# Performance work log

Measured on AMD Instinct MI355X. Metric: run time of the kernel, lower is better.

Reference implementation:

```python
import jax, jax.numpy as jnp
import numpy as np

B, N, C = 32, 512, 1024
H = 16
D = C // H  # 64
MAX_SEQ = 512
BASE = 10000.0


def _rope_tables(n, d):
    # sin/cos tables of shape (n, d//2), matching the torch RoPE buffer math
    position = jnp.arange(n, dtype=jnp.float32)[:, None]
    div_term = jnp.exp(jnp.arange(0, d, 2, dtype=jnp.float32) * (-np.log(BASE) / d))
    ang = position * div_term
    return jnp.sin(ang), jnp.cos(ang)


def _apply_rope(x, sin, cos):
    # x: (B, H, N, D); sin/cos: (N, D//2)
    x1 = x[..., ::2]
    x2 = x[..., 1::2]
    out = jnp.stack([x1 * cos - x2 * sin, x1 * sin + x2 * cos], axis=-1)
    return out.reshape(*x.shape[:-1], -1)


def setup_inputs() -> dict:
    key = jax.random.key(0)
    k1, k2, k3, k4, k5 = jax.random.split(key, 5)
    s = 0.02
    return {
        "x": jax.random.normal(k1, (B, N, C), dtype=jnp.float32),
        "w_qkv": jax.random.normal(k2, (3 * C, C), dtype=jnp.float32) * s,
        "b_qkv": jax.random.normal(k3, (3 * C,), dtype=jnp.float32) * s,
        "w_lepe": jax.random.normal(k4, (C, 1, 3), dtype=jnp.float32) * s,
        "b_lepe": jax.random.normal(k5, (C,), dtype=jnp.float32) * s,
    }


def reference(x, w_qkv, b_qkv, w_lepe, b_lepe):
    b, n, c = x.shape
    scale = 1.0 / np.sqrt(D)
    sin, cos = _rope_tables(n, D)

    # fused QKV projection: (B,N,3C) -> (3,B,H,N,D)
    qkv = (x @ w_qkv.T + b_qkv).reshape(b, n, 3, H, D).transpose(2, 0, 3, 1, 4)
    q, k, v = qkv[0], qkv[1], qkv[2]

    # elu + 1 feature map
    q = jax.nn.elu(q) + 1.0
    k = jax.nn.elu(k) + 1.0

    # RoPE on q/k
    q = _apply_rope(q, sin, cos)
    k = _apply_rope(k, sin, cos)

    # explicit softmax attention
    attn = jnp.einsum('bhnd,bhmd->bhnm', q, k) * scale
    attn = jax.nn.softmax(attn, axis=-1)
    attn_out = jnp.einsum('bhnm,bhmd->bhnd', attn, v)  # (B,H,N,D)
    attn_out = attn_out.transpose(0, 2, 1, 3).reshape(b, n, c)

    # LePE: depthwise conv1d (k=3, pad=1, groups=C) on v reshaped to (B,C,N)
    v_conv = v.transpose(0, 2, 1, 3).reshape(b, n, c).transpose(0, 2, 1)
    lepe = jax.lax.conv_general_dilated(
        v_conv, w_lepe, window_strides=(1,), padding=((1, 1),),
        dimension_numbers=('NCH', 'OIH', 'NCH'), feature_group_count=c,
    ) + b_lepe[None, :, None]
    lepe = lepe.transpose(0, 2, 1)

    return attn_out + lepe
```

## Files before the change

### kernel.cpp

```cpp
#include <hip/hip_runtime.h>
#include <stdint.h>

typedef __attribute__((ext_vector_type(8))) __bf16 bf16x8;
typedef __attribute__((ext_vector_type(4))) float f32x4;
typedef __attribute__((ext_vector_type(8))) unsigned short u16x8;
typedef __attribute__((ext_vector_type(4))) unsigned short u16x4;

#define MFMA16(a, b, c) __builtin_amdgcn_mfma_f32_16x16x32_bf16((a), (b), (c), 0, 0, 0)

__device__ __forceinline__ void glds16(const void* g, void* l) {
  __builtin_amdgcn_global_load_lds(
      (const __attribute__((address_space(1))) void*)(uintptr_t)g,
      (__attribute__((address_space(3))) void*)(uint32_t)(uintptr_t)l,
      16, 0, 0);
}

__device__ __forceinline__ unsigned short f2bf(float f) {
  union { float f; unsigned u; } v; v.f = f;
  unsigned r = v.u + 0x7FFFu + ((v.u >> 16) & 1u);
  return (unsigned short)(r >> 16);
}
__device__ __forceinline__ float bf2f(unsigned short s) {
  union { unsigned u; float f; } v; v.u = ((unsigned)s) << 16;
  return v.f;
}
__device__ __forceinline__ bf16x8 as_bf16x8(u16x8 v) {
  union { u16x8 u; bf16x8 b; } c; c.u = v; return c.b;
}

#define B_ 32
#define N_ 512
#define C_ 1024
#define H_ 16
#define D_ 64
#define K_ C_

__global__ __launch_bounds__(256) void rope_table_kernel(float* __restrict__ sin_t,
                                                         float* __restrict__ cos_t) {
  int idx = blockIdx.x * 256 + threadIdx.x;
  int n = idx >> 5, i = idx & 31;
  float div = expf(-(2.0f * (float)i) * (9.210340371976184f / 64.0f));
  float ang = (float)n * div;
  sin_t[idx] = sinf(ang);
  cos_t[idx] = cosf(ang);
}

__global__ __launch_bounds__(256) void cvt_bf16_kernel(const float* __restrict__ in,
                                                       unsigned short* __restrict__ out,
                                                       int n8) {
  int i = blockIdx.x * blockDim.x + threadIdx.x;
  if (i >= n8) return;
  const float4* p = reinterpret_cast<const float4*>(in) + (size_t)i * 2;
  float4 a = p[0], b = p[1];
  u16x8 o;
  o[0] = f2bf(a.x); o[1] = f2bf(a.y); o[2] = f2bf(a.z); o[3] = f2bf(a.w);
  o[4] = f2bf(b.x); o[5] = f2bf(b.y); o[6] = f2bf(b.z); o[7] = f2bf(b.w);
  *reinterpret_cast<u16x8*>(out + (size_t)i * 8) = o;
}

#define STAGE_T(bi, uu)                                                \
  do {                                                                 \
    _Pragma("unroll") for (int h_ = 0; h_ < 4; ++h_) {                 \
      glds16(aS[h_] + (size_t)(uu) * 64, &lds[bi][h_ * 4096 + t * 8]); \
      glds16(bS[h_] + (size_t)(uu) * 64,                               \
             &lds[bi][16384 + h_ * 4096 + t * 8]);                     \
    }                                                                  \
  } while (0)

__global__ __launch_bounds__(512, 2) void qkv_gemm_kernel(
    const unsigned short* __restrict__ xb, const unsigned short* __restrict__ wb,
    const float* __restrict__ bias,
    unsigned short* __restrict__ Qb, unsigned short* __restrict__ Kb,
    unsigned short* __restrict__ Vtb,
    const float* __restrict__ sin_t, const float* __restrict__ cos_t) {
  __shared__ unsigned short lds[2][32768];
  const int t = threadIdx.x;
  const int wv = t >> 6, l = t & 63;
  const int wr = wv >> 2, wc = wv & 3;
  const int lq = l >> 4, lr = l & 15;

  const int bid = (blockIdx.x & 7) * 96 + (blockIdx.x >> 3);
  const int mBlk = bid / 12, nBlk = bid % 12;
  const int m0 = mBlk * 256, n0 = nBlk * 256;

  const int rl = t >> 3;
  const int cw = ((t & 7) ^ (rl & 7)) * 8;
  const unsigned short* aS[4];
  const unsigned short* bS[4];
#pragma unroll
  for (int h = 0; h < 4; ++h) {
    aS[h] = xb + (size_t)(m0 + h * 64 + rl) * K_ + cw;
    bS[h] = wb + (size_t)(n0 + h * 64 + rl) * K_ + cw;
  }

  const int aBase = (wr * 128 + lr) * 64;
  const int bBase = 16384 + (wc * 64 + lr) * 64;
  int chs[2];
#pragma unroll
  for (int s = 0; s < 2; ++s) chs[s] = ((s * 4 + lq) ^ (lr & 7)) * 8;

  f32x4 acc[8][4] = {};

  STAGE_T(0, 0);
  asm volatile("s_waitcnt vmcnt(0)" ::: "memory");
  __builtin_amdgcn_s_barrier();

  for (int u = 0; u < 16; ++u) {
    const int cur = u & 1;
    const unsigned short* Lc = &lds[cur][0];
    if (u + 1 < 16) STAGE_T(cur ^ 1, u + 1);

    bf16x8 afr[8][2], bfr[4][2];
#pragma unroll
    for (int mf = 0; mf < 8; ++mf)
#pragma unroll
      for (int s = 0; s < 2; ++s)
        afr[mf][s] = *(const bf16x8*)(Lc + aBase + mf * 1024 + chs[s]);
#pragma unroll
    for (int j = 0; j < 4; ++j)
#pragma unroll
      for (int s = 0; s < 2; ++s)
        bfr[j][s] = *(const bf16x8*)(Lc + bBase + j * 1024 + chs[s]);

#pragma unroll
    for (int mf = 0; mf < 8; ++mf)
#pragma unroll
      for (int j = 0; j < 4; ++j)
#pragma unroll
        for (int s = 0; s < 2; ++s)
          acc[mf][j] = MFMA16(afr[mf][s], bfr[j][s], acc[mf][j]);

    asm volatile("s_waitcnt vmcnt(0)\n\ts_barrier" ::: "memory");
  }

  if (n0 >= 2048) {
#pragma unroll
    for (int mf = 0; mf < 8; ++mf) {
#pragma unroll
      for (int j = 0; j < 4; ++j) {
        const int ncol = n0 + wc * 64 + j * 16 + lr;
        const int hh = (ncol & 1023) >> 6;
        const int d = j * 16 + lr;
        const float bias_v = bias[ncol];
        const int m = m0 + wr * 128 + mf * 16 + lq * 4;
        const int bb = m >> 9, nB = m & 511;
        u16x4 vv;
#pragma unroll
        for (int r = 0; r < 4; ++r) vv[r] = f2bf(acc[mf][j][r] + bias_v);
        *(u16x4*)(Vtb + ((size_t)(bb * H_ + hh) * D_ + d) * N_ + nB) = vv;
      }
    }
  } else {
    const bool isQ = (n0 < 1024);
#pragma unroll
    for (int mf = 0; mf < 8; ++mf) {
#pragma unroll
      for (int j = 0; j < 4; ++j) {
        const int ncol = n0 + wc * 64 + j * 16 + lr;
        const int hh = (ncol & 1023) >> 6;
        const int d = ncol & 63;
        const float bias_v = bias[ncol];
#pragma unroll
        for (int r = 0; r < 4; ++r) {
          const int m = m0 + wr * 128 + mf * 16 + lq * 4 + r;
          const int bb = m >> 9, n = m & 511;
          const float val = acc[mf][j][r] + bias_v;
          const float e = val > 0.f ? val + 1.f : expf(val);
          const float partner = __shfl_xor(e, 1);
          const int ip = d >> 1;
          const float sv = sin_t[n * 32 + ip], cv = cos_t[n * 32 + ip];
          float o = (d & 1) ? (partner * sv + e * cv) : (e * cv - partner * sv);
          if (isQ) o *= 0.125f;
          unsigned short* dst = isQ ? Qb : Kb;
          dst[((size_t)(bb * H_ + hh) * N_ + n) * D_ + d] = f2bf(o);
        }
      }
    }
  }
}

__global__ __launch_bounds__(512, 2) void attn_kernel(
    const unsigned short* __restrict__ Qb, const unsigned short* __restrict__ Kb,
    const unsigned short* __restrict__ Vtb,
    const float* __restrict__ w_lepe, const float* __restrict__ b_lepe,
    float* __restrict__ out) {
  __shared__ unsigned short Ks[512 * 64];
  __shared__ unsigned short Vs[64 * 512];
  __shared__ unsigned short Pb[8 * 2 * 1024];
  const int t = threadIdx.x, wv = t >> 6, l = t & 63;
  const int lq = l >> 4, lr = l & 15;
  const int bh = blockIdx.x;
  const int bb = bh >> 4, h = bh & 15;
  const size_t base = (size_t)bh * (N_ * D_);

  {
    const int row8 = t >> 3, ch = t & 7;
#pragma unroll
    for (int c = 0; c < 8; ++c) {
      const int r = c * 64 + row8;
      const int sch = ch ^ (r & 7);
      glds16(Kb + base + (size_t)r * D_ + sch * 8, Ks + c * 4096 + t * 8);
    }
  }
  {
    const int ch = t & 63;
#pragma unroll
    for (int c = 0; c < 8; ++c) {
      const int d = c * 8 + wv;
      const int sch = ch ^ (d & 7);
      glds16(Vtb + base + (size_t)d * N_ + sch * 8, Vs + c * 4096 + t * 8);
    }
  }

  asm volatile("s_waitcnt vmcnt(8)" ::: "memory");
  __builtin_amdgcn_s_barrier();

  unsigned short* PwA = Pb + wv * 2048;
  unsigned short* PwB = PwA + 1024;

#define PWRITE(ccv, Pdst)                                                        \
  do {                                                                           \
    _Pragma("unroll") for (int kl = 0; kl < 4; ++kl) {                           \
      const int kt_ = (ccv) * 4 + kl;                                            \
      u16x4 pk;                                                                  \
      _Pragma("unroll") for (int r = 0; r < 4; ++r) pk[r] = f2bf(s[kt_][r] * inv); \
      const int slot = kl * 2 + (lq >> 1);                                       \
      *(u16x4*)((Pdst) + lr * 64 + ((slot ^ (lr & 7)) << 3) + (lq & 1) * 4) = pk; \
    }                                                                            \
  } while (0)

  bf16x8 qf0 = *(const bf16x8*)(Qb + base + (size_t)(wv * 64 + lr) * D_ + lq * 8);
  bf16x8 qf1 = *(const bf16x8*)(Qb + base + (size_t)(wv * 64 + lr) * D_ + 32 + lq * 8);

  for (int p = 0; p < 4; ++p) {
    const int ql = wv * 64 + p * 16;

    f32x4 s[32];
#pragma unroll
    for (int kt = 0; kt < 32; ++kt) {
      const int r = kt * 16 + lr;
      const int rx = r & 7;
      const unsigned short* kr = Ks + r * 64;
      const bf16x8 kf0 = *(const bf16x8*)(kr + (lq ^ rx) * 8);
      const bf16x8 kf1 = *(const bf16x8*)(kr + ((lq + 4) ^ rx) * 8);
      f32x4 a = {0.f, 0.f, 0.f, 0.f};
      a = MFMA16(kf0, qf0, a);
      a = MFMA16(kf1, qf1, a);
      s[kt] = a;
    }

    if (p < 3) {
      const int qn = ql + 16;
      qf0 = *(const bf16x8*)(Qb + base + (size_t)(qn + lr) * D_ + lq * 8);
      qf1 = *(const bf16x8*)(Qb + base + (size_t)(qn + lr) * D_ + 32 + lq * 8);
    }

    float m = -1e30f;
#pragma unroll
    for (int kt = 0; kt < 32; ++kt)
#pragma unroll
      for (int r = 0; r < 4; ++r) m = fmaxf(m, s[kt][r]);
    m = fmaxf(m, __shfl_xor(m, 16));
    m = fmaxf(m, __shfl_xor(m, 32));
    float su = 0.f;
#pragma unroll
    for (int kt = 0; kt < 32; ++kt)
#pragma unroll
      for (int r = 0; r < 4; ++r) {
        const float pv = __expf(s[kt][r] - m);
        s[kt][r] = pv;
        su += pv;
      }
    su += __shfl_xor(su, 16);
    su += __shfl_xor(su, 32);
    const float inv = 1.0f / su;

    if (p == 0) __syncthreads();

    f32x4 o[4] = {};
    PWRITE(0, PwA);
#pragma unroll
    for (int cc = 0; cc < 8; ++cc) {
      unsigned short* bufC = (cc & 1) ? PwB : PwA;
      unsigned short* bufN = (cc & 1) ? PwA : PwB;
      if (cc < 7) PWRITE(cc + 1, bufN);
      asm volatile("s_waitcnt lgkmcnt(4)" ::: "memory");
#pragma unroll
      for (int w = 0; w < 2; ++w) {
        const u16x8 pr =
            *(const u16x8*)(bufC + lr * 64 + (((w * 4 + lq) ^ (lr & 7)) << 3));
        const bf16x8 pf = as_bf16x8(pr);
        const int ci = cc * 8 + w * 4 + lq;
#pragma unroll
        for (int j2 = 0; j2 < 4; j2++) {
          const int dr = j2 * 16 + lr;
          const bf16x8 vf = *(const bf16x8*)(Vs + dr * 512 + ((ci ^ (dr & 7)) << 3));
          o[j2] = MFMA16(pf, vf, o[j2]);
        }
      }
    }

#pragma unroll
    for (int j2 = 0; j2 < 4; j2++) {
      const int d = j2 * 16 + lr;
      const int c = h * 64 + d;
      const float w0 = w_lepe[c * 3 + 0], w1 = w_lepe[c * 3 + 1], w2 = w_lepe[c * 3 + 2];
      const float bl = b_lepe[c];
      const int dx = d & 7;
#pragma unroll
      for (int r = 0; r < 4; r++) {
        const int n = ql + lq * 4 + r;
        float vm1 = 0.f, vp1 = 0.f;
        if (n > 0) {
          const int nn = n - 1;
          vm1 = bf2f(Vs[d * 512 + (((nn >> 3) ^ dx) << 3) + (nn & 7)]);
        }
        const float v0 = bf2f(Vs[d * 512 + (((n >> 3) ^ dx) << 3) + (n & 7)]);
        if (n < 511) {
          const int nn = n + 1;
          vp1 = bf2f(Vs[d * 512 + (((nn >> 3) ^ dx) << 3) + (nn & 7)]);
        }
        const float lepe = vm1 * w0 + v0 * w1 + vp1 * w2 + bl;
        out[((size_t)(bb * N_ + n)) * C_ + c] = o[j2][r] + lepe;
      }
    }
  }
#undef PWRITE
}

extern "C" void kernel_launch(void* const* d_in, const int* in_sizes, int n_in,
                              void* d_out, int out_size, void* d_ws, size_t ws_size,
                              hipStream_t stream) {
  (void)in_sizes; (void)n_in; (void)out_size; (void)ws_size;
  const float* x = (const float*)d_in[0];
  const float* w_qkv = (const float*)d_in[1];
  const float* b_qkv = (const float*)d_in[2];
  const float* w_lepe = (const float*)d_in[3];
  const float* b_lepe = (const float*)d_in[4];
  float* out = (float*)d_out;

  unsigned short* ws = (unsigned short*)d_ws;
  unsigned short* xb = ws;
  unsigned short* wb = xb + 16777216;
  unsigned short* Qb = wb + 3145728;
  unsigned short* Kb = Qb + 16777216;
  unsigned short* Vtb = Kb + 16777216;
  float* sin_t = (float*)(Vtb + 16777216);
  float* cos_t = sin_t + 16384;

  rope_table_kernel<<<64, 256, 0, stream>>>(sin_t, cos_t);
  cvt_bf16_kernel<<<(16777216 / 8 + 255) / 256, 256, 0, stream>>>(x, xb, 16777216 / 8);
  cvt_bf16_kernel<<<(3145728 / 8 + 255) / 256, 256, 0, stream>>>(w_qkv, wb, 3145728 / 8);
  qkv_gemm_kernel<<<768, 512, 0, stream>>>(xb, wb, b_qkv, Qb, Kb, Vtb, sin_t, cos_t);
  attn_kernel<<<512, 512, 0, stream>>>(Qb, Kb, Vtb, w_lepe, b_lepe, out);
}
```

Before: 237.4 us.

## Halve GEMM K-tile to raise occupancy; split softmax reductions into parallel chains

The QKV GEMM K-step tile drops from 64 to 32, which halves LDS use per block and requires a new staging layout and swizzle. Launch bounds rise to 4 blocks per SM so more blocks can be resident at once. This doubles the number of loop iterations and barriers. Separately, the softmax max and sum reductions in attention now use 8 independent accumulators instead of one serial chain, which shortens the dependency latency.

```diff
diff --git a/kernel.cpp b/kernel.cpp
--- a/kernel.cpp
+++ b/kernel.cpp
@@ -58,22 +58,21 @@
   *reinterpret_cast<u16x8*>(out + (size_t)i * 8) = o;
 }
 
-#define STAGE_T(bi, uu)                                                \
-  do {                                                                 \
-    _Pragma("unroll") for (int h_ = 0; h_ < 4; ++h_) {                 \
-      glds16(aS[h_] + (size_t)(uu) * 64, &lds[bi][h_ * 4096 + t * 8]); \
-      glds16(bS[h_] + (size_t)(uu) * 64,                               \
-             &lds[bi][16384 + h_ * 4096 + t * 8]);                     \
-    }                                                                  \
+#define STAGE_T(bi, uu)                                                 \
+  do {                                                                  \
+    _Pragma("unroll") for (int h_ = 0; h_ < 2; ++h_) {                  \
+      glds16(aS[h_] + (uu) * 32, &lds[bi][h_ * 4096 + t * 8]);          \
+      glds16(bS[h_] + (uu) * 32, &lds[bi][8192 + h_ * 4096 + t * 8]);   \
+    }                                                                   \
   } while (0)
 
-__global__ __launch_bounds__(512, 2) void qkv_gemm_kernel(
+__global__ __launch_bounds__(512, 4) void qkv_gemm_kernel(
     const unsigned short* __restrict__ xb, const unsigned short* __restrict__ wb,
     const float* __restrict__ bias,
     unsigned short* __restrict__ Qb, unsigned short* __restrict__ Kb,
     unsigned short* __restrict__ Vtb,
     const float* __restrict__ sin_t, const float* __restrict__ cos_t) {
-  __shared__ unsigned short lds[2][32768];
+  __shared__ unsigned short lds[2][16384];
   const int t = threadIdx.x;
   const int wv = t >> 6, l = t & 63;
   const int wr = wv >> 2, wc = wv & 3;
@@ -83,21 +82,19 @@
   const int mBlk = bid / 12, nBlk = bid % 12;
   const int m0 = mBlk * 256, n0 = nBlk * 256;
 
-  const int rl = t >> 3;
-  const int cw = ((t & 7) ^ (rl & 7)) * 8;
-  const unsigned short* aS[4];
-  const unsigned short* bS[4];
-#pragma unroll
-  for (int h = 0; h < 4; ++h) {
-    aS[h] = xb + (size_t)(m0 + h * 64 + rl) * K_ + cw;
-    bS[h] = wb + (size_t)(n0 + h * 64 + rl) * K_ + cw;
-  }
-
-  const int aBase = (wr * 128 + lr) * 64;
-  const int bBase = 16384 + (wc * 64 + lr) * 64;
-  int chs[2];
-#pragma unroll
-  for (int s = 0; s < 2; ++s) chs[s] = ((s * 4 + lq) ^ (lr & 7)) * 8;
+  const int rl2 = t >> 2;
+  const int cw2 = ((t & 3) ^ ((rl2 >> 1) & 3)) * 8;
+  const unsigned short* aS[2];
+  const unsigned short* bS[2];
+#pragma unroll
+  for (int h = 0; h < 2; ++h) {
+    aS[h] = xb + (size_t)(m0 + h * 128 + rl2) * K_ + cw2;
+    bS[h] = wb + (size_t)(n0 + h * 128 + rl2) * K_ + cw2;
+  }
+
+  const int chs = (lq ^ ((lr >> 1) & 3)) * 8;
+  const int aBase = (wr * 128 + lr) * 32 + chs;
+  const int bBase = 8192 + (wc * 64 + lr) * 32 + chs;
 
   f32x4 acc[8][4] = {};
 
@@ -105,30 +102,24 @@
   asm volatile("s_waitcnt vmcnt(0)" ::: "memory");
   __builtin_amdgcn_s_barrier();
 
-  for (int u = 0; u < 16; ++u) {
+  for (int u = 0; u < 32; ++u) {
     const int cur = u & 1;
     const unsigned short* Lc = &lds[cur][0];
-    if (u + 1 < 16) STAGE_T(cur ^ 1, u + 1);
-
-    bf16x8 afr[8][2], bfr[4][2];
+    if (u + 1 < 32) STAGE_T(cur ^ 1, u + 1);
+
+    bf16x8 afr[8], bfr[4];
 #pragma unroll
     for (int mf = 0; mf < 8; ++mf)
-#pragma unroll
-      for (int s = 0; s < 2; ++s)
-        afr[mf][s] = *(const bf16x8*)(Lc + aBase + mf * 1024 + chs[s]);
+      afr[mf] = *(const bf16x8*)(Lc + aBase + mf * 512);
 #pragma unroll
     for (int j = 0; j < 4; ++j)
-#pragma unroll
-      for (int s = 0; s < 2; ++s)
-        bfr[j][s] = *(const bf16x8*)(Lc + bBase + j * 1024 + chs[s]);
+      bfr[j] = *(const bf16x8*)(Lc + bBase + j * 512);
 
 #pragma unroll
     for (int mf = 0; mf < 8; ++mf)
 #pragma unroll
       for (int j = 0; j < 4; ++j)
-#pragma unroll
-        for (int s = 0; s < 2; ++s)
-          acc[mf][j] = MFMA16(afr[mf][s], bfr[j][s], acc[mf][j]);
+        acc[mf][j] = MFMA16(afr[mf], bfr[j], acc[mf][j]);
 
     asm volatile("s_waitcnt vmcnt(0)\n\ts_barrier" ::: "memory");
   }
@@ -255,22 +246,38 @@
       qf1 = *(const bf16x8*)(Qb + base + (size_t)(qn + lr) * D_ + 32 + lq * 8);
     }
 
-    float m = -1e30f;
+    float macc[8];
+#pragma unroll
+    for (int i = 0; i < 8; ++i) macc[i] = -1e30f;
 #pragma unroll
     for (int kt = 0; kt < 32; ++kt)
 #pragma unroll
-      for (int r = 0; r < 4; ++r) m = fmaxf(m, s[kt][r]);
+      for (int r = 0; r < 4; ++r)
+        macc[(kt & 1) * 4 + r] = fmaxf(macc[(kt & 1) * 4 + r], s[kt][r]);
+#pragma unroll
+    for (int i = 0; i < 4; ++i) macc[i] = fmaxf(macc[i], macc[i + 4]);
+    macc[0] = fmaxf(macc[0], macc[1]);
+    macc[2] = fmaxf(macc[2], macc[3]);
+    float m = fmaxf(macc[0], macc[2]);
     m = fmaxf(m, __shfl_xor(m, 16));
     m = fmaxf(m, __shfl_xor(m, 32));
-    float su = 0.f;
+
+    float sacc[8];
+#pragma unroll
+    for (int i = 0; i < 8; ++i) sacc[i] = 0.f;
 #pragma unroll
     for (int kt = 0; kt < 32; ++kt)
 #pragma unroll
       for (int r = 0; r < 4; ++r) {
         const float pv = __expf(s[kt][r] - m);
         s[kt][r] = pv;
-        su += pv;
-      }
+        sacc[(kt & 1) * 4 + r] += pv;
+      }
+#pragma unroll
+    for (int i = 0; i < 4; ++i) sacc[i] += sacc[i + 4];
+    sacc[0] += sacc[1];
+    sacc[2] += sacc[3];
+    float su = sacc[0] + sacc[2];
     su += __shfl_xor(su, 16);
     su += __shfl_xor(su, 32);
     const float inv = 1.0f / su;
```

Measured after the change: 774.6 us. 3.26x slower.
